# Kernel tuning notes

Hardware: AMD Instinct MI355X
Metric: run time of the kernel (lower is better)

The kernel has to match this reference:

```python
import jax, jax.numpy as jnp
import numpy as np

# YOLOv5-style NMS + scale_coords constants
CONF_THRES = 0.25
IOU_THRES = 0.45
MAX_DET = 300      # max detections kept per image
TOPK = 1024        # candidate pool fed to greedy NMS (static for jit)
MAX_WH = 4096.0    # class offset for class-aware NMS
IMG1 = (640.0, 640.0)   # shape1: letterboxed network input (h, w)
IMG0 = (720.0, 1280.0)  # shape0: original image (h, w)


def xywh2xyxy(x):
    xy, wh = x[..., :2], x[..., 2:4] * 0.5
    return jnp.concatenate([xy - wh, xy + wh], axis=-1)


def iou_one_to_many(b, B):
    # b: [4], B: [K,4] in xyxy
    lt = jnp.maximum(b[:2], B[:, :2])
    rb = jnp.minimum(b[2:], B[:, 2:])
    wh = jnp.clip(rb - lt, 0.0)
    inter = wh[:, 0] * wh[:, 1]
    a1 = (b[2] - b[0]) * (b[3] - b[1])
    a2 = (B[:, 2] - B[:, 0]) * (B[:, 3] - B[:, 1])
    return inter / (a1 + a2 - inter + 1e-9)


def nms_single(pred):
    # pred: [N, 85] = xywh, obj, 80 class scores
    obj = pred[:, 4]
    conf_all = obj[:, None] * pred[:, 5:]          # obj * cls conf
    conf = conf_all.max(axis=-1)
    cls = jnp.argmax(conf_all, axis=-1).astype(pred.dtype)
    boxes = xywh2xyxy(pred[:, :4])
    valid = (obj > CONF_THRES) & (conf > CONF_THRES)
    sc = jnp.where(valid, conf, -1.0)
    sc_top, idx = jax.lax.top_k(sc, TOPK)          # candidate pool
    b = boxes[idx]                                  # [K,4]
    c = cls[idx]                                    # [K]
    off = b + c[:, None] * MAX_WH                   # class-aware offset boxes

    def body(i, state):
        s, sel, selv = state
        p = jnp.argmax(s)
        pv = s[p] > 0.0
        iou = iou_one_to_many(off[p], off)
        s = jnp.where(iou > IOU_THRES, -1.0, s).at[p].set(-1.0)
        return s, sel.at[i].set(p), selv.at[i].set(pv)

    init = (sc_top, jnp.zeros(MAX_DET, jnp.int32), jnp.zeros(MAX_DET, bool))
    _, sel, selv = jax.lax.fori_loop(0, MAX_DET, body, init)

    det = jnp.concatenate(
        [b[sel], sc_top[sel][:, None], c[sel][:, None]], axis=-1)  # [max_det,6]
    return jnp.where(selv[:, None], det, 0.0)


def scale_coords(coords):
    # undo letterbox: IMG1 (h1,w1) -> IMG0 (h0,w0)
    h1, w1 = IMG1
    h0, w0 = IMG0
    gain = min(h1 / h0, w1 / w0)
    pad_x = (w1 - w0 * gain) / 2.0
    pad_y = (h1 - h0 * gain) / 2.0
    x1 = jnp.clip((coords[..., 0] - pad_x) / gain, 0.0, w0)
    y1 = jnp.clip((coords[..., 1] - pad_y) / gain, 0.0, h0)
    x2 = jnp.clip((coords[..., 2] - pad_x) / gain, 0.0, w0)
    y2 = jnp.clip((coords[..., 3] - pad_y) / gain, 0.0, h0)
    return jnp.stack([x1, y1, x2, y2], axis=-1)


def setup_inputs() -> dict:
    key = jax.random.key(0)
    kxy, kwh, kobj, kcls = jax.random.split(key, 4)
    B, N, NC = 16, 25200, 80
    xy = jax.random.uniform(kxy, (B, N, 2), jnp.float32) * 640.0
    wh = jax.random.uniform(kwh, (B, N, 2), jnp.float32) * 160.0 + 2.0
    obj = jax.random.uniform(kobj, (B, N, 1), jnp.float32)
    cls = jax.random.uniform(kcls, (B, N, NC), jnp.float32)
    pred = jnp.concatenate([xy, wh, obj, cls], axis=-1)  # [B, N, 85]
    return {"pred": pred}


def reference(pred):
    det = jax.vmap(nms_single)(pred)                 # [B, max_det, 6]
    boxes = scale_coords(det[..., :4])
    # columns: x1,y1,x2,y2 (rescaled), score, label
    return jnp.concatenate([boxes, det[..., 4:]], axis=-1)
```

## Files before the change

### kernel.cpp

```cpp
#include <hip/hip_runtime.h>
#include <stdint.h>

#define N_CAND 25200
#define NB 16
#define ROW 85
#define TK 1024
#define MAXDET 300
#define CAP 2048
#define BITS_LO 0x3E800000u

typedef unsigned long long u64;
typedef unsigned int u32;

struct u64x2 { u64 x, y; };

static __device__ __forceinline__ u64 u64min(u64 a, u64 b) { return a < b ? a : b; }
static __device__ __forceinline__ u64 u64max(u64 a, u64 b) { return a > b ? a : b; }

__global__ __launch_bounds__(256, 8) void score_kernel(const float* __restrict__ pred,
                                                       u64* __restrict__ keys)
{
#pragma clang fp contract(off)
    __shared__ float tile[64 * ROW];
    const int tid = threadIdx.x;
    const int row0 = blockIdx.x * 64;
    const float4* src = (const float4*)(pred + (size_t)row0 * ROW);
    float4* dst = (float4*)tile;
#pragma unroll
    for (int i = 0; i < 6; ++i) {
        int idx = tid + (i << 8);
        if (idx < (64 * ROW) / 4) {
            __builtin_amdgcn_global_load_lds(
                (const __attribute__((address_space(1))) void*)(src + idx),
                (__attribute__((address_space(3))) void*)(dst + idx),
                16, 0, 0);
        }
    }
    __syncthreads();

    const int r = tid >> 2, sub = tid & 3;
    const float* rowp = tile + r * ROW;
    const float obj = rowp[4];
    const int base = 5 + sub * 20;
    float bv = obj * rowp[base];
    int bi = base - 5;
#pragma unroll
    for (int c = 1; c < 20; ++c) {
        float p = obj * rowp[base + c];
        if (p > bv) { bv = p; bi = base - 5 + c; }
    }
#pragma unroll
    for (int off = 1; off <= 2; off <<= 1) {
        float ov = __shfl_xor(bv, off, 64);
        int   oi = __shfl_xor(bi, off, 64);
        if (ov > bv || (ov == bv && oi < bi)) { bv = ov; bi = oi; }
    }
    if (sub == 0) {
        int w = row0 + r;
        u32 n = (u32)w % N_CAND;
        u64 key = 0;
        if (obj > 0.25f && bv > 0.25f)
            key = ((u64)__float_as_uint(bv) << 32) | (((u64)(25199u - n)) << 7) | (u32)bi;
        keys[w] = key;
    }
}

__global__ __launch_bounds__(1024) void topk_kernel(const float* __restrict__ pred,
                                                    const u64* __restrict__ keys,
                                                    float4* __restrict__ soaA,
                                                    float4* __restrict__ soaB)
{
#pragma clang fp contract(off)
    __shared__ u64 sbuf[CAP];
    __shared__ u32 histA[2048];
    __shared__ u32 histB[2048];
    __shared__ u32 s_t;
    __shared__ int s_fb;

    const int tid = threadIdx.x;
    const int b = blockIdx.x;
    const u64* kb = keys + (size_t)b * N_CAND;
    const u64x2* kb2 = (const u64x2*)kb;
    const float* pb = pred + (size_t)b * N_CAND * ROW;

    for (int i = tid; i < 2048; i += 1024) histA[i] = 0;
    for (int i = tid; i < CAP; i += 1024) sbuf[i] = 0ull;
    if (tid == 0) { s_t = 0; s_fb = 0; }
    __syncthreads();

    for (int p = tid; p < N_CAND / 2; p += 1024) {
        u64x2 kk = kb2[p];
        u32 bits0 = (u32)(kk.x >> 32);
        if (bits0) {
            int bin = (int)((bits0 - BITS_LO) >> 13);
            bin = bin < 0 ? 0 : (bin > 2047 ? 2047 : bin);
            atomicAdd(&histA[bin], 1u);
        }
        u32 bits1 = (u32)(kk.y >> 32);
        if (bits1) {
            int bin = (int)((bits1 - BITS_LO) >> 13);
            bin = bin < 0 ? 0 : (bin > 2047 ? 2047 : bin);
            atomicAdd(&histA[bin], 1u);
        }
    }
    __syncthreads();

    u32* srcp = histA; u32* dstp = histB;
    for (int step = 1; step < 2048; step <<= 1) {
        for (int i = tid; i < 2048; i += 1024)
            dstp[i] = srcp[i] + ((i + step < 2048) ? srcp[i + step] : 0u);
        __syncthreads();
        u32* t = srcp; srcp = dstp; dstp = t;
    }
    for (int i = tid; i < 2048; i += 1024) {
        u32 S = srcp[i];
        if (S >= TK && (i == 2047 || srcp[i + 1] < TK)) s_t = (u32)i;
    }
    __syncthreads();
    const int t = (int)s_t;
    const u32 thr = BITS_LO + ((u32)t << 13);

    for (int i = tid; i < 2048; i += 1024) {
        u32 base = (i < 2047) ? srcp[i + 1] : 0u;
        dstp[i] = base;
        if (i >= t && (srcp[i] - base) > 64u) s_fb = 1;
    }
    __syncthreads();

    for (int p = tid; p < N_CAND / 2; p += 1024) {
        u64x2 kk = kb2[p];
        u32 bits0 = (u32)(kk.x >> 32);
        if (bits0 >= thr) {
            int bin = (int)((bits0 - BITS_LO) >> 13);
            bin = bin < 0 ? 0 : (bin > 2047 ? 2047 : bin);
            u32 pos = atomicAdd(&dstp[bin], 1u);
            if (pos < CAP) sbuf[pos] = kk.x;
        }
        u32 bits1 = (u32)(kk.y >> 32);
        if (bits1 >= thr) {
            int bin = (int)((bits1 - BITS_LO) >> 13);
            bin = bin < 0 ? 0 : (bin > 2047 ? 2047 : bin);
            u32 pos = atomicAdd(&dstp[bin], 1u);
            if (pos < CAP) sbuf[pos] = kk.y;
        }
    }
    __syncthreads();

    if (!s_fb) {
        const int wave = tid >> 6, lane = tid & 63;
        for (int bin = t + wave; bin < 2048; bin += 16) {
            u32 base = (bin < 2047) ? srcp[bin + 1] : 0u;
            u32 end = srcp[bin]; if (end > CAP) end = CAP;
            if (end <= base + 1) continue;
            u32 cnt_b = end - base;
            u64 v = (lane < (int)cnt_b) ? sbuf[base + lane] : 0ull;
#pragma unroll
            for (int k2 = 2; k2 <= 64; k2 <<= 1) {
                for (int j = k2 >> 1; j > 0; j >>= 1) {
                    u64 p = __shfl_xor(v, j, 64);
                    const bool up = ((lane & k2) == 0);
                    const bool low = ((lane & j) == 0);
                    v = (up == low) ? u64max(v, p) : u64min(v, p);
                }
            }
            if (lane < (int)cnt_b) sbuf[base + lane] = v;
        }
        __syncthreads();
    } else {
        const int E0 = tid << 1;
        u64 e0 = sbuf[E0], e1 = sbuf[E0 + 1];
        for (int k = 2; k <= CAP; k <<= 1) {
            for (int j = k >> 1; j > 0; j >>= 1) {
                const bool asc = ((E0 & k) == 0);
                if (j >= 128) {
                    __syncthreads();
                    sbuf[E0] = e0; sbuf[E0 + 1] = e1;
                    __syncthreads();
                    u64 p0 = sbuf[E0 ^ j], p1 = sbuf[(E0 + 1) ^ j];
                    const bool low = ((E0 & j) == 0);
                    e0 = (asc == low) ? u64min(e0, p0) : u64max(e0, p0);
                    e1 = (asc == low) ? u64min(e1, p1) : u64max(e1, p1);
                } else if (j >= 2) {
                    const int l = j >> 1;
                    u64 p0 = __shfl_xor(e0, l, 64);
                    u64 p1 = __shfl_xor(e1, l, 64);
                    const bool low = ((E0 & j) == 0);
                    e0 = (asc == low) ? u64min(e0, p0) : u64max(e0, p0);
                    e1 = (asc == low) ? u64min(e1, p1) : u64max(e1, p1);
                } else {
                    u64 mn = u64min(e0, e1), mx = u64max(e0, e1);
                    e0 = asc ? mn : mx;
                    e1 = asc ? mx : mn;
                }
            }
        }
        __syncthreads();
        sbuf[E0] = e0; sbuf[E0 + 1] = e1;
        __syncthreads();
    }

    {
        const int i = tid;
        u64 k = sbuf[s_fb ? (CAP - 1 - i) : i];
        u32 bits = (u32)(k >> 32);
        float4 A, Bv;
        if (bits) {
            u32 lo = (u32)k;
            u32 n = 25199u - (lo >> 7);
            float c = (float)(lo & 127u);
            const float* rp = pb + (size_t)n * ROW;
            float x = rp[0], y = rp[1], ww = rp[2], hh = rp[3];
            float hw = ww * 0.5f, hv = hh * 0.5f;
            float x1 = x - hw, y1 = y - hv, x2 = x + hw, y2 = y + hv;
            float offc = c * 4096.0f;
            float area = ((x2 + offc) - (x1 + offc)) * ((y2 + offc) - (y1 + offc));
            A = make_float4(x1, y1, x2, y2);
            Bv = make_float4(area, __uint_as_float(bits), c, 0.0f);
        } else {
            A = make_float4(0.0f, 0.0f, 0.0f, 0.0f);
            Bv = make_float4(0.0f, -1.0f, 0.0f, 0.0f);
        }
        soaA[b * TK + i] = A;
        soaB[b * TK + i] = Bv;
    }
}

__global__ __launch_bounds__(512) void mask_kernel(const float4* __restrict__ soaA,
                                                   const float4* __restrict__ soaB,
                                                   u64* __restrict__ masks)
{
#pragma clang fp contract(off)
    __shared__ float qx1[TK], qy1[TK], qx2[TK], qy2[TK], qar[TK];
    const int tid = threadIdx.x;
    const int b = blockIdx.y;
    const int rbase = blockIdx.x * 32;
    const int wi = rbase >> 6;
    for (int i = tid; i < TK; i += 512) {
        float4 A = soaA[b * TK + i];
        float4 Bv = soaB[b * TK + i];
        float off = Bv.z * 4096.0f;
        qx1[i] = A.x + off; qy1[i] = A.y + off;
        qx2[i] = A.z + off; qy2[i] = A.w + off;
        qar[i] = Bv.x;
    }
    __syncthreads();

    const int wave = tid >> 6, lane = tid & 63;
    for (int rr = 0; rr < 4; ++rr) {
        int i = rbase + (wave << 2) + rr;
        float px1 = qx1[i], py1 = qy1[i];
        float px2 = qx2[i], py2 = qy2[i];
        float parea = qar[i];
        u64 myword = 0;
        for (int word = wi; word < 16; ++word) {
            int j = (word << 6) + lane;
            float ltx = fmaxf(px1, qx1[j]), lty = fmaxf(py1, qy1[j]);
            float rbx = fminf(px2, qx2[j]), rby = fminf(py2, qy2[j]);
            float w2 = fmaxf(rbx - ltx, 0.0f), h2 = fmaxf(rby - lty, 0.0f);
            float inter = w2 * h2;
            float iou = inter / (parea + qar[j] - inter + 1e-9f);
            u64 m = __ballot(iou > 0.45f);
            if (lane == word) myword = m;
        }
        if (lane >= wi && lane < 16) masks[((size_t)(b * TK + i) << 4) + lane] = myword;
    }
}

__global__ __launch_bounds__(64) void sweep_kernel(const float4* __restrict__ soaA,
                                                   const float4* __restrict__ soaB,
                                                   const u64* __restrict__ masks,
                                                   float* __restrict__ out)
{
#pragma clang fp contract(off)
    __shared__ int sel[MAXDET];
    const int lane = threadIdx.x;
    const int b = blockIdx.x;
    const u64* mb = masks + ((size_t)(b * TK) << 4);

    float sv[16];
#pragma unroll
    for (int k = 0; k < 16; ++k)
        sv[k] = soaB[b * TK + (k << 6) + lane].y;
    int nv = TK;
    bool found = false;
#pragma unroll
    for (int k = 0; k < 16; ++k) {
        u64 m = __ballot(sv[k] > 0.0f);
        if (!found && m != ~0ull) { nv = (k << 6) + (int)__builtin_ctzll(~m); found = true; }
    }

    u64 removed = 0;
    int nsel = 0;
    bool done = (nv == 0);
    const int li = lane & 15;

    u64 cur[8], nxt[8];
#pragma unroll
    for (int r = 0; r < 8; ++r) cur[r] = mb[((size_t)r << 4) + li];

    for (int c = 0; c < 128 && !done; ++c) {
        int nb0 = (c + 1) << 3;
#pragma unroll
        for (int r = 0; r < 8; ++r) {
            int i2 = nb0 + r; if (i2 > TK - 1) i2 = TK - 1;
            nxt[r] = mb[((size_t)i2 << 4) + li];
        }
#pragma unroll
        for (int r = 0; r < 8; ++r) {
            int i = (c << 3) + r;
            if (!done && i < nv) {
                u64 wv = __shfl(removed, i >> 6, 64);
                if (!((wv >> (i & 63)) & 1ull)) {
                    if (lane == 0) sel[nsel] = i;
                    removed |= cur[r];
                    ++nsel;
                    if (nsel == MAXDET) done = true;
                }
            } else if (i >= nv) done = true;
        }
#pragma unroll
        for (int r = 0; r < 8; ++r) cur[r] = nxt[r];
    }
    __syncthreads();

    for (int r = lane; r < MAXDET; r += 64) {
        float* o = out + ((size_t)b * MAXDET + r) * 6;
        if (r < nsel) {
            int p = sel[r];
            float4 A = soaA[b * TK + p];
            float4 Bv = soaB[b * TK + p];
            float X1 = (A.x - 0.0f) / 0.5f;
            float Y1 = (A.y - 140.0f) / 0.5f;
            float X2 = (A.z - 0.0f) / 0.5f;
            float Y2 = (A.w - 140.0f) / 0.5f;
            X1 = fminf(fmaxf(X1, 0.0f), 1280.0f);
            Y1 = fminf(fmaxf(Y1, 0.0f), 720.0f);
            X2 = fminf(fmaxf(X2, 0.0f), 1280.0f);
            Y2 = fminf(fmaxf(Y2, 0.0f), 720.0f);
            o[0] = X1; o[1] = Y1; o[2] = X2; o[3] = Y2;
            o[4] = Bv.y; o[5] = Bv.z;
        } else {
            o[0] = 0.0f; o[1] = 0.0f; o[2] = 0.0f;
            o[3] = 0.0f; o[4] = 0.0f; o[5] = 0.0f;
        }
    }
}

extern "C" void kernel_launch(void* const* d_in, const int* in_sizes, int n_in,
                              void* d_out, int out_size, void* d_ws, size_t ws_size,
                              hipStream_t stream)
{
    const float* pred = (const float*)d_in[0];
    float* out = (float*)d_out;

    u64* keys = (u64*)d_ws;
    u64* masks = (u64*)d_ws;
    float4* soaA = (float4*)((char*)d_ws + 3225600);
    float4* soaB = (float4*)((char*)d_ws + 3225600 + 262144);

    score_kernel<<<(NB * N_CAND) / 64, 256, 0, stream>>>(pred, keys);
    topk_kernel<<<NB, 1024, 0, stream>>>(pred, keys, soaA, soaB);
    mask_kernel<<<dim3(32, NB), 512, 0, stream>>>(soaA, soaB, masks);
    sweep_kernel<<<NB, 64, 0, stream>>>(soaA, soaB, masks, out);
}
```

Measured before the change: 109.7 us.

## Split per-image score histogram into separate multi-block kernel

Moves the coarse score histogram out of the single-block-per-image top-k kernel into a new kernel that uses 4 blocks per image, each building a partial histogram over a chunk of keys. The top-k kernel then just sums the four partial histograms. This spreads the key scan across more compute units instead of 16 blocks, at the cost of an extra kernel launch and a global round-trip for the partial histograms.

```diff
diff --git a/kernel.cpp b/kernel.cpp
--- a/kernel.cpp
+++ b/kernel.cpp
@@ -8,6 +8,7 @@
 #define MAXDET 300
 #define CAP 2048
 #define BITS_LO 0x3E800000u
+#define CHUNK 6300
 
 typedef unsigned long long u64;
 typedef unsigned int u32;
@@ -65,8 +66,39 @@
     }
 }
 
+__global__ __launch_bounds__(256) void hist_kernel(const u64* __restrict__ keys,
+                                                   u32* __restrict__ ghist)
+{
+    __shared__ u32 h[2048];
+    const int tid = threadIdx.x;
+    const int c = blockIdx.x;
+    const int b = blockIdx.y;
+    for (int i = tid; i < 2048; i += 256) h[i] = 0;
+    __syncthreads();
+    const u64x2* src = (const u64x2*)(keys + (size_t)b * N_CAND + c * CHUNK);
+    for (int p = tid; p < CHUNK / 2; p += 256) {
+        u64x2 kk = src[p];
+        u32 bits0 = (u32)(kk.x >> 32);
+        if (bits0) {
+            int bin = (int)((bits0 - BITS_LO) >> 13);
+            bin = bin < 0 ? 0 : (bin > 2047 ? 2047 : bin);
+            atomicAdd(&h[bin], 1u);
+        }
+        u32 bits1 = (u32)(kk.y >> 32);
+        if (bits1) {
+            int bin = (int)((bits1 - BITS_LO) >> 13);
+            bin = bin < 0 ? 0 : (bin > 2047 ? 2047 : bin);
+            atomicAdd(&h[bin], 1u);
+        }
+    }
+    __syncthreads();
+    u32* dst = ghist + ((size_t)((b << 2) + c) << 11);
+    for (int i = tid; i < 2048; i += 256) dst[i] = h[i];
+}
+
 __global__ __launch_bounds__(1024) void topk_kernel(const float* __restrict__ pred,
                                                     const u64* __restrict__ keys,
+                                                    const u32* __restrict__ ghist,
                                                     float4* __restrict__ soaA,
                                                     float4* __restrict__ soaB)
 {
@@ -83,25 +115,15 @@
     const u64x2* kb2 = (const u64x2*)kb;
     const float* pb = pred + (size_t)b * N_CAND * ROW;
 
-    for (int i = tid; i < 2048; i += 1024) histA[i] = 0;
     for (int i = tid; i < CAP; i += 1024) sbuf[i] = 0ull;
     if (tid == 0) { s_t = 0; s_fb = 0; }
-    __syncthreads();
-
-    for (int p = tid; p < N_CAND / 2; p += 1024) {
-        u64x2 kk = kb2[p];
-        u32 bits0 = (u32)(kk.x >> 32);
-        if (bits0) {
-            int bin = (int)((bits0 - BITS_LO) >> 13);
-            bin = bin < 0 ? 0 : (bin > 2047 ? 2047 : bin);
-            atomicAdd(&histA[bin], 1u);
-        }
-        u32 bits1 = (u32)(kk.y >> 32);
-        if (bits1) {
-            int bin = (int)((bits1 - BITS_LO) >> 13);
-            bin = bin < 0 ? 0 : (bin > 2047 ? 2047 : bin);
-            atomicAdd(&histA[bin], 1u);
-        }
+
+    for (int i = tid; i < 2048; i += 1024) {
+        u32 s = 0;
+#pragma unroll
+        for (int c = 0; c < 4; ++c)
+            s += ghist[((size_t)((b << 2) + c) << 11) + i];
+        histA[i] = s;
     }
     __syncthreads();
 
@@ -357,9 +379,11 @@
     u64* masks = (u64*)d_ws;
     float4* soaA = (float4*)((char*)d_ws + 3225600);
     float4* soaB = (float4*)((char*)d_ws + 3225600 + 262144);
+    u32* ghist = (u32*)((char*)d_ws + 3749888);
 
     score_kernel<<<(NB * N_CAND) / 64, 256, 0, stream>>>(pred, keys);
-    topk_kernel<<<NB, 1024, 0, stream>>>(pred, keys, soaA, soaB);
+    hist_kernel<<<dim3(4, NB), 256, 0, stream>>>(keys, ghist);
+    topk_kernel<<<NB, 1024, 0, stream>>>(pred, keys, ghist, soaA, soaB);
     mask_kernel<<<dim3(32, NB), 512, 0, stream>>>(soaA, soaB, masks);
     sweep_kernel<<<NB, 64, 0, stream>>>(soaA, soaB, masks, out);
 }
```

Measured after the change: 114.5 us. +4.4%, slower.
